# Kernel tuning notes

Measured on AMD Instinct MI355X. Metric: run time of the kernel, lower is better.

## Reference

```python
import jax, jax.numpy as jnp
import numpy as np

WINDOW = 8  # window_size from init; keys per query = WINDOW + 1 (causal, inclusive of self)


def setup_inputs() -> dict:
    key = jax.random.key(0)
    ks = jax.random.split(key, 5)
    S, D, R = 32768, 1024, 256
    x = jax.random.normal(ks[0], (S, D), dtype=jnp.float32)
    Wq = jax.random.normal(ks[1], (D, R), dtype=jnp.float32) / D ** 0.5
    Wk = jax.random.normal(ks[2], (D, R), dtype=jnp.float32) / D ** 0.5
    Wv = jax.random.normal(ks[3], (D, R), dtype=jnp.float32) / D ** 0.5
    Wo = jax.random.normal(ks[4], (R, D), dtype=jnp.float32) / R ** 0.5
    bq = jnp.zeros((R,), dtype=jnp.float32)
    bk = jnp.zeros((R,), dtype=jnp.float32)
    bv = jnp.zeros((R,), dtype=jnp.float32)
    bo = jnp.zeros((D,), dtype=jnp.float32)
    return {"x": x, "Wq": Wq, "Wk": Wk, "Wv": Wv, "Wo": Wo,
            "bq": bq, "bk": bk, "bv": bv, "bo": bo}


def reference(x, Wq, Wk, Wv, Wo, bq, bk, bv, bo):
    S, D = x.shape
    R = Wq.shape[1]
    W = WINDOW + 1  # keys per query
    Q = x @ Wq + bq  # [S, R]
    K = x @ Wk + bk  # [S, R]
    V = x @ Wv + bv  # [S, R]
    # For query i, attend to positions i-WINDOW .. i (clamped at 0).
    offs = jnp.arange(-WINDOW, 1)                      # [W]
    idx = jnp.arange(S)[:, None] + offs[None, :]       # [S, W]
    valid = idx >= 0
    idxc = jnp.clip(idx, 0, S - 1)
    Kw = K[idxc]                                       # [S, W, R]
    Vw = V[idxc]                                       # [S, W, R]
    scores = jnp.einsum('sr,swr->sw', Q, Kw) / (R ** 0.5)
    scores = jnp.where(valid, scores, -jnp.inf)
    attn = jax.nn.softmax(scores, axis=-1)             # [S, W]
    ctx = jnp.einsum('sw,swr->sr', attn, Vw)           # [S, R]
    return ctx @ Wo + bo                               # [S, D]
```

## Files before the change

kernel.cpp:

```cpp
#include <hip/hip_runtime.h>
#include <stdint.h>


typedef __attribute__((ext_vector_type(8))) short short8;
typedef __attribute__((ext_vector_type(4))) float floatx4;

typedef __attribute__((address_space(1))) const void global_cv;
typedef __attribute__((address_space(3))) void lds_v;

__device__ __forceinline__ float b2f(unsigned short u) {
  union { float f; uint32_t i; } v; v.i = ((uint32_t)u) << 16; return v.f;
}
__device__ __forceinline__ unsigned short f2b(float f) {
  union { float f; uint32_t i; } v; v.f = f;
  uint32_t x = v.i;
  return (unsigned short)((x + 0x7FFFu + ((x >> 16) & 1u)) >> 16);
}
__device__ __forceinline__ uint32_t pack2bf(float a, float b) {
  uint32_t ua = (__float_as_uint(a) + 0x8000u) >> 16;
  uint32_t ub = (__float_as_uint(b) + 0x8000u) & 0xFFFF0000u;
  return ua | ub;
}

__device__ __forceinline__ void async16(const unsigned short* g, unsigned short* s) {
  __builtin_amdgcn_global_load_lds((global_cv*)g, (lds_v*)s, 16, 0, 0);
}

__device__ __forceinline__ void storeC(unsigned short* C, size_t idx, float v) {
  C[idx] = f2b(v);
}
__device__ __forceinline__ void storeC(float* C, size_t idx, float v) {
  C[idx] = v;
}

__global__ __launch_bounds__(256) void cvt_x(
    const float* __restrict__ x, unsigned short* __restrict__ xb, int n8)
{
  const int stride = gridDim.x * blockDim.x;
  for (int i = blockIdx.x * blockDim.x + threadIdx.x; i < n8; i += stride) {
    const float4 u = ((const float4*)x)[2 * i];
    const float4 v = ((const float4*)x)[2 * i + 1];
    uint4 pk;
    pk.x = pack2bf(u.x, u.y); pk.y = pack2bf(u.z, u.w);
    pk.z = pack2bf(v.x, v.y); pk.w = pack2bf(v.z, v.w);
    ((uint4*)xb)[i] = pk;
  }
}

template <typename CT, int NTB>
__global__ __launch_bounds__(256) void gemm_bt(
    const unsigned short* __restrict__ A,
    const unsigned short* __restrict__ Bt,
    const float* __restrict__ bias,
    CT* __restrict__ C,
    int K, int lda, int ldb, int ldc)
{
  __shared__ __align__(16) unsigned short sA[3][128 * 32];
  __shared__ __align__(16) unsigned short sB[3][128 * 32];

  const int tid = threadIdx.x;
  const int w   = tid >> 6;
  const int l   = tid & 63;
  const int l15 = l & 15;
  const int q   = l >> 4;

  const int bt  = blockIdx.x;
  const int xcd = bt & 7;
  const int j_  = bt >> 3;
  const int n0  = (j_ % NTB) * 128;
  const int m0  = ((j_ / NTB) * 8 + xcd) * 128;

  const int wm  = (w >> 1) * 64;
  const int wn  = (w & 1) * 64;

  floatx4 acc[4][4];
  #pragma unroll
  for (int i = 0; i < 4; ++i)
    #pragma unroll
    for (int j = 0; j < 4; ++j)
      #pragma unroll
      for (int t = 0; t < 4; ++t) acc[i][j][t] = 0.f;

  const int sr  = l >> 2;
  const int pc_ = l & 3;
  const int lc  = pc_ ^ ((sr >> 1) & 3);
  const unsigned short* Asrc[2];
  const unsigned short* Bsrc[2];
  #pragma unroll
  for (int j = 0; j < 2; ++j) {
    const int rr = (w * 2 + j) * 16 + sr;
    Asrc[j] = A  + (size_t)(m0 + rr) * lda + lc * 8;
    Bsrc[j] = Bt + (size_t)(n0 + rr) * ldb + lc * 8;
  }

  const int fq   = (q ^ ((l15 >> 1) & 3)) * 8;
  const int aoff = (wm + l15) * 32 + fq;
  const int boff = (wn + l15) * 32 + fq;

  const int KT = K >> 5;

  #define STAGE(k0, b)                                                   \
    {                                                                    \
      _Pragma("unroll")                                                  \
      for (int j = 0; j < 2; ++j) {                                      \
        async16(Asrc[j] + (k0), &sA[b][(w * 2 + j) * 512]);              \
        async16(Bsrc[j] + (k0), &sB[b][(w * 2 + j) * 512]);              \
      }                                                                  \
    }

  STAGE(0, 0);
  STAGE(32, 1);
  asm volatile("s_waitcnt vmcnt(4)" ::: "memory");
  __builtin_amdgcn_s_barrier();

  int bc = 0;
  for (int t = 0; t < KT; ++t) {
    const int k2 = (t + 2) << 5;
    const int bs = (bc == 0) ? 2 : bc - 1;
    if (k2 < K) STAGE(k2, bs);

    short8 af[4], bf[4];
    #pragma unroll
    for (int mt = 0; mt < 4; ++mt)
      af[mt] = *(const short8*)(&sA[bc][aoff + mt * 512]);
    #pragma unroll
    for (int nt = 0; nt < 4; ++nt)
      bf[nt] = *(const short8*)(&sB[bc][boff + nt * 512]);

    #pragma unroll
    for (int mt = 0; mt < 4; ++mt)
      #pragma unroll
      for (int nt = 0; nt < 4; ++nt)
        acc[mt][nt] = __builtin_amdgcn_mfma_f32_16x16x32_bf16(
            af[mt], bf[nt], acc[mt][nt], 0, 0, 0);

    if (k2 < K) {
      asm volatile("s_waitcnt vmcnt(4)" ::: "memory");
    } else {
      asm volatile("s_waitcnt vmcnt(0)" ::: "memory");
    }
    if (t + 1 < KT) __builtin_amdgcn_s_barrier();
    bc = (bc == 2) ? 0 : bc + 1;
  }
  #undef STAGE

  #pragma unroll
  for (int nt = 0; nt < 4; ++nt) {
    const int col = n0 + wn + nt * 16 + l15;
    const float bs = bias[col];
    #pragma unroll
    for (int mt = 0; mt < 4; ++mt) {
      const int rbase = m0 + wm + mt * 16 + q * 4;
      #pragma unroll
      for (int r = 0; r < 4; ++r)
        storeC(C, (size_t)(rbase + r) * ldc + col, acc[mt][nt][r] + bs);
    }
  }
}

__global__ __launch_bounds__(256) void attn_win(unsigned short* QKV)
{
  const int l   = threadIdx.x & 63;
  const int grp = l >> 4;
  const int p   = l & 15;
  const int i   = blockIdx.x * 16 + (threadIdx.x >> 6) * 4 + grp;

  unsigned short* qrow = QKV + (size_t)i * 768 + p * 16;
  float qf[16];
  {
    const short8 v0 = *(const short8*)(qrow);
    const short8 v1 = *(const short8*)(qrow + 8);
    #pragma unroll
    for (int t = 0; t < 8; ++t) {
      qf[t]     = b2f((unsigned short)v0[t]);
      qf[8 + t] = b2f((unsigned short)v1[t]);
    }
  }

  float sc[9];
  #pragma unroll
  for (int wd = 0; wd < 9; ++wd) {
    const int j = i - 8 + wd;
    if (j >= 0) {
      const unsigned short* krow = QKV + (size_t)j * 768 + 256 + p * 16;
      const short8 v0 = *(const short8*)(krow);
      const short8 v1 = *(const short8*)(krow + 8);
      float d = 0.f;
      #pragma unroll
      for (int t = 0; t < 8; ++t) {
        d += qf[t]     * b2f((unsigned short)v0[t]);
        d += qf[8 + t] * b2f((unsigned short)v1[t]);
      }
      d += __shfl_xor(d, 8, 64);
      d += __shfl_xor(d, 4, 64);
      d += __shfl_xor(d, 2, 64);
      d += __shfl_xor(d, 1, 64);
      sc[wd] = d * 0.0625f;
    } else {
      sc[wd] = -1e30f;
    }
  }

  float mx = sc[0];
  #pragma unroll
  for (int wd = 1; wd < 9; ++wd) mx = fmaxf(mx, sc[wd]);
  float e[9], s = 0.f;
  #pragma unroll
  for (int wd = 0; wd < 9; ++wd) { e[wd] = __expf(sc[wd] - mx); s += e[wd]; }
  const float inv = 1.0f / s;

  float acc[16];
  #pragma unroll
  for (int t = 0; t < 16; ++t) acc[t] = 0.f;
  #pragma unroll
  for (int wd = 0; wd < 9; ++wd) {
    const int j = i - 8 + wd;
    if (j >= 0) {
      const unsigned short* vrow = QKV + (size_t)j * 768 + 512 + p * 16;
      const short8 v0 = *(const short8*)(vrow);
      const short8 v1 = *(const short8*)(vrow + 8);
      #pragma unroll
      for (int t = 0; t < 8; ++t) {
        acc[t]     += e[wd] * b2f((unsigned short)v0[t]);
        acc[8 + t] += e[wd] * b2f((unsigned short)v1[t]);
      }
    }
  }
  short8 o0, o1;
  #pragma unroll
  for (int t = 0; t < 8; ++t) {
    o0[t] = (short)f2b(acc[t] * inv);
    o1[t] = (short)f2b(acc[8 + t] * inv);
  }
  *(short8*)(qrow)     = o0;
  *(short8*)(qrow + 8) = o1;
}

__global__ __launch_bounds__(256) void prep_w(
    const float* __restrict__ Wq, const float* __restrict__ Wk,
    const float* __restrict__ Wv, const float* __restrict__ Wo,
    const float* __restrict__ bq, const float* __restrict__ bk,
    const float* __restrict__ bv, const float* __restrict__ bo,
    unsigned short* __restrict__ Wt,
    unsigned short* __restrict__ Wot,
    float* __restrict__ bias1,
    float* __restrict__ bias2)
{
  const int tt = blockIdx.x;
  if (tt < 1024) {
    __shared__ float tile[32][33];
    const float* src; unsigned short* dst; int N, Kd, k0, n0;
    if (tt < 768) {
      const int s = tt >> 8;
      const int r = tt & 255;
      src = (s == 0) ? Wq : (s == 1) ? Wk : Wv;
      N = 256; Kd = 1024;
      k0 = (r & 31) * 32;
      n0 = (r >> 5) * 32;
      dst = Wt + (size_t)s * 256 * 1024;
    } else {
      const int r = tt - 768;
      src = Wo; N = 1024; Kd = 256;
      k0 = (r & 7) * 32;
      n0 = (r >> 3) * 32;
      dst = Wot;
    }
    const int t  = threadIdx.x;
    const int rr = t >> 3;
    const int c4 = (t & 7) * 4;
    const float4 v = *(const float4*)(src + (size_t)(k0 + rr) * N + n0 + c4);
    tile[rr][c4 + 0] = v.x; tile[rr][c4 + 1] = v.y;
    tile[rr][c4 + 2] = v.z; tile[rr][c4 + 3] = v.w;
    __syncthreads();
    ushort4 o;
    o.x = f2b(tile[c4 + 0][rr]); o.y = f2b(tile[c4 + 1][rr]);
    o.z = f2b(tile[c4 + 2][rr]); o.w = f2b(tile[c4 + 3][rr]);
    *(ushort4*)(dst + (size_t)(n0 + rr) * Kd + k0 + c4) = o;
  } else {
    for (int c = threadIdx.x; c < 1792; c += 256) {
      if (c < 768)
        bias1[c] = (c < 256) ? bq[c] : (c < 512) ? bk[c - 256] : bv[c - 512];
      else
        bias2[c - 768] = bo[c - 768];
    }
  }
}

extern "C" void kernel_launch(void* const* d_in, const int* in_sizes, int n_in,
                              void* d_out, int out_size, void* d_ws, size_t ws_size,
                              hipStream_t stream) {
  const float* x  = (const float*)d_in[0];
  const float* Wq = (const float*)d_in[1];
  const float* Wk = (const float*)d_in[2];
  const float* Wv = (const float*)d_in[3];
  const float* Wo = (const float*)d_in[4];
  const float* bq = (const float*)d_in[5];
  const float* bk = (const float*)d_in[6];
  const float* bv = (const float*)d_in[7];
  const float* bo = (const float*)d_in[8];
  float* out = (float*)d_out;

  unsigned short* ws    = (unsigned short*)d_ws;
  unsigned short* Wt    = ws;
  unsigned short* Wot   = Wt  + 786432;
  float*          bias1 = (float*)(Wot + 262144);
  float*          bias2 = bias1 + 768;
  unsigned short* QKV   = (unsigned short*)(bias2 + 1024);
  unsigned short* xb;
  const size_t need = 119544832;
  if (ws_size >= need) xb = QKV + 25165824;
  else                 xb = (unsigned short*)d_out;

  prep_w<<<1025, 256, 0, stream>>>(Wq, Wk, Wv, Wo, bq, bk, bv, bo,
                                   Wt, Wot, bias1, bias2);

  cvt_x<<<2048, 256, 0, stream>>>(x, xb, 32768 * 1024 / 8);

  gemm_bt<unsigned short, 6><<<1536, 256, 0, stream>>>(
      xb, Wt, bias1, QKV, 1024, 1024, 1024, 768);

  attn_win<<<2048, 256, 0, stream>>>(QKV);

  gemm_bt<float, 8><<<2048, 256, 0, stream>>>(
      QKV, Wot, bias2, out, 256, 768, 256, 1024);
}
```

Before: 364.2 us.

## Enlarge GEMM tiles to 256x128 with BK=64 and fuse x conversion into prep

The GEMM kernel now runs 512 threads per block on a 256x128 output tile with a 64-wide K step. It uses an XOR-swizzled LDS layout, a barrier at the top of each iteration and s_setprio around the MFMA block. This is meant to improve operand reuse and cut the number of barriers per unit of K. The x fp32-to-bf16 conversion is merged into the weight-prep kernel to save one launch. In exchange, LDS use grows to about 144KB per block, which limits occupancy, and the block count is halved.

New measurement: 373.9 us. 2.7% more time.

```diff
diff --git a/kernel.cpp b/kernel.cpp
--- a/kernel.cpp
+++ b/kernel.cpp
@@ -33,30 +33,16 @@
   C[idx] = v;
 }
 
-__global__ __launch_bounds__(256) void cvt_x(
-    const float* __restrict__ x, unsigned short* __restrict__ xb, int n8)
-{
-  const int stride = gridDim.x * blockDim.x;
-  for (int i = blockIdx.x * blockDim.x + threadIdx.x; i < n8; i += stride) {
-    const float4 u = ((const float4*)x)[2 * i];
-    const float4 v = ((const float4*)x)[2 * i + 1];
-    uint4 pk;
-    pk.x = pack2bf(u.x, u.y); pk.y = pack2bf(u.z, u.w);
-    pk.z = pack2bf(v.x, v.y); pk.w = pack2bf(v.z, v.w);
-    ((uint4*)xb)[i] = pk;
-  }
-}
-
 template <typename CT, int NTB>
-__global__ __launch_bounds__(256) void gemm_bt(
+__global__ __launch_bounds__(512) void gemm_dp(
     const unsigned short* __restrict__ A,
     const unsigned short* __restrict__ Bt,
     const float* __restrict__ bias,
     CT* __restrict__ C,
     int K, int lda, int ldb, int ldc)
 {
-  __shared__ __align__(16) unsigned short sA[3][128 * 32];
-  __shared__ __align__(16) unsigned short sB[3][128 * 32];
+  __shared__ __align__(16) unsigned short sA[3][256 * 64];
+  __shared__ __align__(16) unsigned short sB[3][128 * 64];
 
   const int tid = threadIdx.x;
   const int w   = tid >> 6;
@@ -68,7 +54,7 @@
   const int xcd = bt & 7;
   const int j_  = bt >> 3;
   const int n0  = (j_ % NTB) * 128;
-  const int m0  = ((j_ / NTB) * 8 + xcd) * 128;
+  const int m0  = ((j_ / NTB) * 8 + xcd) * 256;
 
   const int wm  = (w >> 1) * 64;
   const int wn  = (w & 1) * 64;
@@ -81,65 +67,66 @@
       #pragma unroll
       for (int t = 0; t < 4; ++t) acc[i][j][t] = 0.f;
 
-  const int sr  = l >> 2;
-  const int pc_ = l & 3;
-  const int lc  = pc_ ^ ((sr >> 1) & 3);
-  const unsigned short* Asrc[2];
-  const unsigned short* Bsrc[2];
-  #pragma unroll
-  for (int j = 0; j < 2; ++j) {
-    const int rr = (w * 2 + j) * 16 + sr;
-    Asrc[j] = A  + (size_t)(m0 + rr) * lda + lc * 8;
-    Bsrc[j] = Bt + (size_t)(n0 + rr) * ldb + lc * 8;
-  }
-
-  const int fq   = (q ^ ((l15 >> 1) & 3)) * 8;
-  const int aoff = (wm + l15) * 32 + fq;
-  const int boff = (wn + l15) * 32 + fq;
-
-  const int KT = K >> 5;
-
-  #define STAGE(k0, b)                                                   \
-    {                                                                    \
-      _Pragma("unroll")                                                  \
-      for (int j = 0; j < 2; ++j) {                                      \
-        async16(Asrc[j] + (k0), &sA[b][(w * 2 + j) * 512]);              \
-        async16(Bsrc[j] + (k0), &sB[b][(w * 2 + j) * 512]);              \
-      }                                                                  \
-    }
+  const int srow8 = l >> 3;
+  const int lc    = ((l & 7) ^ srow8) * 8;
+  const unsigned short* Asrc = A  + (size_t)(m0 + w * 32 + srow8) * lda + lc;
+  const unsigned short* Bsrc = Bt + (size_t)(n0 + w * 16 + srow8) * ldb + lc;
+
+  #define STAGE(k2, b)                                                        \
+    {                                                                         \
+      _Pragma("unroll")                                                       \
+      for (int j = 0; j < 4; ++j)                                             \
+        async16(Asrc + (size_t)(j * 8) * lda + (k2),                          \
+                &sA[b][(w * 32 + j * 8) * 64]);                               \
+      _Pragma("unroll")                                                       \
+      for (int j = 0; j < 2; ++j)                                             \
+        async16(Bsrc + (size_t)(j * 8) * ldb + (k2),                          \
+                &sB[b][(w * 16 + j * 8) * 64]);                               \
+    }
+
+  const int rx   = l15 & 7;
+  const int pc0  = (q ^ rx) * 8;
+  const int arow = (wm + l15) * 64;
+  const int brow = (wn + l15) * 64;
+
+  const int KT = K >> 6;
 
   STAGE(0, 0);
-  STAGE(32, 1);
-  asm volatile("s_waitcnt vmcnt(4)" ::: "memory");
-  __builtin_amdgcn_s_barrier();
+  STAGE(64, 1);
 
   int bc = 0;
   for (int t = 0; t < KT; ++t) {
-    const int k2 = (t + 2) << 5;
-    const int bs = (bc == 0) ? 2 : bc - 1;
-    if (k2 < K) STAGE(k2, bs);
-
-    short8 af[4], bf[4];
-    #pragma unroll
-    for (int mt = 0; mt < 4; ++mt)
-      af[mt] = *(const short8*)(&sA[bc][aoff + mt * 512]);
-    #pragma unroll
-    for (int nt = 0; nt < 4; ++nt)
-      bf[nt] = *(const short8*)(&sB[bc][boff + nt * 512]);
-
-    #pragma unroll
-    for (int mt = 0; mt < 4; ++mt)
+    if (t + 1 < KT)
+      asm volatile("s_waitcnt vmcnt(6)\n\ts_barrier" ::: "memory");
+    else
+      asm volatile("s_waitcnt vmcnt(0)\n\ts_barrier" ::: "memory");
+
+    const int k2 = (t + 2) << 6;
+    const int b2 = (bc == 0) ? 2 : bc - 1;
+    if (k2 < K) STAGE(k2, b2);
+
+    short8 af[2][4], bf[2][4];
+    #pragma unroll
+    for (int kk = 0; kk < 2; ++kk) {
+      const int pcs = pc0 ^ (kk << 5);
+      #pragma unroll
+      for (int mt = 0; mt < 4; ++mt)
+        af[kk][mt] = *(const short8*)(&sA[bc][arow + mt * 1024 + pcs]);
       #pragma unroll
       for (int nt = 0; nt < 4; ++nt)
-        acc[mt][nt] = __builtin_amdgcn_mfma_f32_16x16x32_bf16(
-            af[mt], bf[nt], acc[mt][nt], 0, 0, 0);
-
-    if (k2 < K) {
-      asm volatile("s_waitcnt vmcnt(4)" ::: "memory");
-    } else {
-      asm volatile("s_waitcnt vmcnt(0)" ::: "memory");
-    }
-    if (t + 1 < KT) __builtin_amdgcn_s_barrier();
+        bf[kk][nt] = *(const short8*)(&sB[bc][brow + nt * 1024 + pcs]);
+    }
+    __builtin_amdgcn_s_setprio(1);
+    #pragma unroll
+    for (int kk = 0; kk < 2; ++kk)
+      #pragma unroll
+      for (int mt = 0; mt < 4; ++mt)
+        #pragma unroll
+        for (int nt = 0; nt < 4; ++nt)
+          acc[mt][nt] = __builtin_amdgcn_mfma_f32_16x16x32_bf16(
+              af[kk][mt], bf[kk][nt], acc[mt][nt], 0, 0, 0);
+    __builtin_amdgcn_s_setprio(0);
+
     bc = (bc == 2) ? 0 : bc + 1;
   }
   #undef STAGE
@@ -236,30 +223,32 @@
   *(short8*)(qrow + 8) = o1;
 }
 
-__global__ __launch_bounds__(256) void prep_w(
+__global__ __launch_bounds__(256) void prep_all(
     const float* __restrict__ Wq, const float* __restrict__ Wk,
     const float* __restrict__ Wv, const float* __restrict__ Wo,
     const float* __restrict__ bq, const float* __restrict__ bk,
     const float* __restrict__ bv, const float* __restrict__ bo,
+    const float* __restrict__ x,
     unsigned short* __restrict__ Wt,
     unsigned short* __restrict__ Wot,
     float* __restrict__ bias1,
-    float* __restrict__ bias2)
+    float* __restrict__ bias2,
+    unsigned short* __restrict__ xb)
 {
-  const int tt = blockIdx.x;
-  if (tt < 1024) {
+  const int bb = blockIdx.x;
+  if (bb < 1024) {
     __shared__ float tile[32][33];
     const float* src; unsigned short* dst; int N, Kd, k0, n0;
-    if (tt < 768) {
-      const int s = tt >> 8;
-      const int r = tt & 255;
+    if (bb < 768) {
+      const int s = bb >> 8;
+      const int r = bb & 255;
       src = (s == 0) ? Wq : (s == 1) ? Wk : Wv;
       N = 256; Kd = 1024;
       k0 = (r & 31) * 32;
       n0 = (r >> 5) * 32;
       dst = Wt + (size_t)s * 256 * 1024;
     } else {
-      const int r = tt - 768;
+      const int r = bb - 768;
       src = Wo; N = 1024; Kd = 256;
       k0 = (r & 7) * 32;
       n0 = (r >> 3) * 32;
@@ -276,12 +265,23 @@
     o.x = f2b(tile[c4 + 0][rr]); o.y = f2b(tile[c4 + 1][rr]);
     o.z = f2b(tile[c4 + 2][rr]); o.w = f2b(tile[c4 + 3][rr]);
     *(ushort4*)(dst + (size_t)(n0 + rr) * Kd + k0 + c4) = o;
-  } else {
+  } else if (bb == 1024) {
     for (int c = threadIdx.x; c < 1792; c += 256) {
       if (c < 768)
         bias1[c] = (c < 256) ? bq[c] : (c < 512) ? bk[c - 256] : bv[c - 512];
       else
         bias2[c - 768] = bo[c - 768];
+    }
+  } else {
+    const int n8 = 32768 * 1024 / 8;
+    const int stride = 2048 * 256;
+    for (int i = (bb - 1025) * 256 + threadIdx.x; i < n8; i += stride) {
+      const float4 u = ((const float4*)x)[2 * i];
+      const float4 v = ((const float4*)x)[2 * i + 1];
+      uint4 pk;
+      pk.x = pack2bf(u.x, u.y); pk.y = pack2bf(u.z, u.w);
+      pk.z = pack2bf(v.x, v.y); pk.w = pack2bf(v.z, v.w);
+      ((uint4*)xb)[i] = pk;
     }
   }
 }
@@ -311,16 +311,14 @@
   if (ws_size >= need) xb = QKV + 25165824;
   else                 xb = (unsigned short*)d_out;
 
-  prep_w<<<1025, 256, 0, stream>>>(Wq, Wk, Wv, Wo, bq, bk, bv, bo,
-                                   Wt, Wot, bias1, bias2);
-
-  cvt_x<<<2048, 256, 0, stream>>>(x, xb, 32768 * 1024 / 8);
-
-  gemm_bt<unsigned short, 6><<<1536, 256, 0, stream>>>(
+  prep_all<<<3073, 256, 0, stream>>>(Wq, Wk, Wv, Wo, bq, bk, bv, bo, x,
+                                     Wt, Wot, bias1, bias2, xb);
+
+  gemm_dp<unsigned short, 6><<<768, 512, 0, stream>>>(
       xb, Wt, bias1, QKV, 1024, 1024, 1024, 768);
 
   attn_win<<<2048, 256, 0, stream>>>(QKV);
 
-  gemm_bt<float, 8><<<2048, 256, 0, stream>>>(
+  gemm_dp<float, 8><<<1024, 512, 0, stream>>>(
       QKV, Wot, bias2, out, 256, 768, 256, 1024);
 }
```
